# Optimization experiments

Hardware: AMD Instinct MI355X
Metric: run time of the kernel (lower is better)

The kernel has to match this reference:

```python
import jax, jax.numpy as jnp
import numpy as np

B, T, D = 2, 2048, 1024
N_HEADS = 16
HEAD_DIM = D // N_HEADS
HIDDEN = 4 * D
LN_EPS = 1e-6  # flax LayerNorm default


def apply_rotary_pos_emb(x, positions):
    # x: (B, T, H, head_dim); positions: (T,)
    head_dim = x.shape[-1]
    inv_freq = 1.0 / 10000 ** (jnp.arange(0, head_dim, 2).astype(jnp.float32) / head_dim)
    freqs = jnp.outer(positions.astype(jnp.float32), inv_freq)  # (T, head_dim//2)
    cos_emb = jnp.cos(freqs)[None, :, None, :]
    sin_emb = jnp.sin(freqs)[None, :, None, :]
    x1 = x[..., : head_dim // 2]
    x2 = x[..., head_dim // 2 :]
    return jnp.concatenate([x1 * cos_emb - x2 * sin_emb,
                            x1 * sin_emb + x2 * cos_emb], axis=-1)


def layernorm(x, scale, bias):
    mu = jnp.mean(x, axis=-1, keepdims=True)
    var = jnp.mean(jnp.square(x - mu), axis=-1, keepdims=True)
    return (x - mu) * jax.lax.rsqrt(var + LN_EPS) * scale + bias


def setup_inputs() -> dict:
    key = jax.random.key(0)
    ks = jax.random.split(key, 8)
    lecun = lambda k, shape: jax.random.normal(k, shape, jnp.float32) * (1.0 / np.sqrt(shape[0]))
    x = jax.random.normal(ks[0], (B, T, D), jnp.float32)
    positions = jnp.arange(T, dtype=jnp.int32)
    mask = jnp.tril(jnp.ones((T, T), dtype=bool))[None, None]  # causal (1,1,T,T)
    return {
        "x": x,
        "positions": positions,
        "mask": mask,
        "ln1_scale": jnp.ones((D,), jnp.float32),
        "ln1_bias": jnp.zeros((D,), jnp.float32),
        "w_qkv": lecun(ks[1], (D, 3 * D)),
        "w_o": lecun(ks[2], (D, D)),
        "ln2_scale": jnp.ones((D,), jnp.float32),
        "ln2_bias": jnp.zeros((D,), jnp.float32),
        "w1": lecun(ks[3], (D, HIDDEN)),
        "b1": jnp.zeros((HIDDEN,), jnp.float32),
        "w2": lecun(ks[4], (HIDDEN, D)),
        "b2": jnp.zeros((D,), jnp.float32),
    }


def reference(x, positions, mask, ln1_scale, ln1_bias, w_qkv, w_o,
              ln2_scale, ln2_bias, w1, b1, w2, b2):
    h = layernorm(x, ln1_scale, ln1_bias)
    qkv = h @ w_qkv  # (B,T,3D)
    qkv = qkv.reshape(B, T, 3, N_HEADS, HEAD_DIM)
    q, k, v = jnp.moveaxis(qkv, 2, 0)  # each (B,T,H,hd)
    q = apply_rotary_pos_emb(q, positions)
    k = apply_rotary_pos_emb(k, positions)
    q = jnp.transpose(q, (0, 2, 1, 3))  # (B,H,T,hd)
    k = jnp.transpose(k, (0, 2, 1, 3))
    v = jnp.transpose(v, (0, 2, 1, 3))
    scale = 1.0 / jnp.sqrt(jnp.float32(HEAD_DIM))
    attn_weights = jnp.einsum('bhqd,bhkd->bhqk', q, k) * scale
    attn_weights = jnp.where(mask, attn_weights, -1e10)
    attn_weights = jax.nn.softmax(attn_weights, axis=-1)
    h = jnp.einsum('bhqk,bhkd->bhqd', attn_weights, v)
    h = jnp.transpose(h, (0, 2, 1, 3)).reshape(B, T, D)
    h = h @ w_o
    x = x + h
    h = layernorm(x, ln2_scale, ln2_bias)
    h = jax.nn.gelu(h @ w1 + b1)  # approximate gelu, matching flax nn.gelu default
    h = h @ w2 + b2
    return x + h
```

## Files before the change

kernel.cpp:

```cpp
#include <hip/hip_runtime.h>


typedef __bf16 bf16_t;
typedef bf16_t bf16x8 __attribute__((ext_vector_type(8)));
typedef float f32x4 __attribute__((ext_vector_type(4)));

#define M_ROWS 4096
#define DMODEL 1024
#define TSEQ   2048
#define NHEAD  16
#define HDIM   64

__device__ __forceinline__ ushort f2bf(float f) {
  union { float f; unsigned u; } v; v.f = f;
  unsigned r = (v.u + 0x7fffu + ((v.u >> 16) & 1u)) >> 16;
  return (ushort)r;
}
__device__ __forceinline__ float bf2f(ushort u) {
  union { unsigned u; float f; } v; v.u = ((unsigned)u) << 16;
  return v.f;
}
__device__ __forceinline__ unsigned cvt_pk_bf16(float a, float b) {
  unsigned r;
  asm("v_cvt_pk_bf16_f32 %0, %1, %2" : "=v"(r) : "v"(a), "v"(b));
  return r;
}
__device__ __forceinline__ void gload_lds16(const void* g, void* l) {
  __builtin_amdgcn_global_load_lds(
      (const __attribute__((address_space(1))) unsigned*)g,
      (__attribute__((address_space(3))) unsigned*)l, 16, 0, 0);
}
__device__ __forceinline__ f32x4 mfma16(bf16x8 a, bf16x8 b, f32x4 c) {
  return __builtin_amdgcn_mfma_f32_16x16x32_bf16(a, b, c, 0, 0, 0);
}
__device__ __forceinline__ float gelu_f(float x) {
  float y = 0.7978845608028654f * (x + 0.044715f * x * x * x);
  float e = __expf(2.0f * y);
  float t = 1.0f - 2.0f / (e + 1.0f);
  return 0.5f * x * (1.0f + t);
}

__global__ __launch_bounds__(256)
void transpose_bf16(const float* __restrict__ src, ushort* __restrict__ dst,
                    int K, int N) {
  __shared__ float t[32][33];
  int n0 = blockIdx.x * 32, k0 = blockIdx.y * 32;
  int tx = threadIdx.x & 31, ty = threadIdx.x >> 5;
#pragma unroll
  for (int i = 0; i < 4; i++) {
    int k = ty + i * 8;
    t[k][tx] = src[(size_t)(k0 + k) * N + n0 + tx];
  }
  __syncthreads();
#pragma unroll
  for (int i = 0; i < 4; i++) {
    int nn = ty + i * 8;
    dst[(size_t)(n0 + nn) * K + k0 + tx] = f2bf(t[tx][nn]);
  }
}

__global__ __launch_bounds__(256)
void ln_kernel(const float* __restrict__ x, const float* __restrict__ sc,
               const float* __restrict__ bi, ushort* __restrict__ out) {
  int row = blockIdx.x;
  int tid = threadIdx.x;
  const float4 v = *(const float4*)&x[(size_t)row * DMODEL + tid * 4];
  float s = v.x + v.y + v.z + v.w;
  float s2 = v.x * v.x + v.y * v.y + v.z * v.z + v.w * v.w;
#pragma unroll
  for (int off = 32; off > 0; off >>= 1) {
    s += __shfl_down(s, off);
    s2 += __shfl_down(s2, off);
  }
  __shared__ float red[8];
  int lane = tid & 63, w = tid >> 6;
  if (lane == 0) { red[w * 2] = s; red[w * 2 + 1] = s2; }
  __syncthreads();
  float S = red[0] + red[2] + red[4] + red[6];
  float S2 = red[1] + red[3] + red[5] + red[7];
  float mu = S * (1.0f / DMODEL);
  float var = S2 * (1.0f / DMODEL) - mu * mu;
  float rs = rsqrtf(var + 1e-6f);
  float4 scv = *(const float4*)&sc[tid * 4];
  float4 biv = *(const float4*)&bi[tid * 4];
  ushort4 o;
  o.x = f2bf((v.x - mu) * rs * scv.x + biv.x);
  o.y = f2bf((v.y - mu) * rs * scv.y + biv.y);
  o.z = f2bf((v.z - mu) * rs * scv.z + biv.z);
  o.w = f2bf((v.w - mu) * rs * scv.w + biv.w);
  *(ushort4*)&out[(size_t)row * DMODEL + tid * 4] = o;
}

__global__ __launch_bounds__(256)
void rope_table(const int* __restrict__ positions, float2* __restrict__ tab) {
  int i = blockIdx.x * 256 + threadIdx.x;
  int t = i >> 5, f = i & 31;
  float inv = __expf(-(float)f * (1.0f / 32.0f) * 9.210340371976184f);
  float a = (float)positions[t] * inv;
  tab[i] = make_float2(cosf(a), sinf(a));
}

__global__ __launch_bounds__(256)
void rope_apply(const ushort* __restrict__ qkv, const float2* __restrict__ tab,
                ushort* __restrict__ Q, ushort* __restrict__ Kd,
                ushort* __restrict__ VT) {
  __shared__ ushort vt[64][66];
  int t0 = blockIdx.x * 64;
  int bh = blockIdx.y;
  int b = bh >> 4, h = bh & 15;
  int f = threadIdx.x & 31, tg = threadIdx.x >> 5;
#pragma unroll
  for (int i = 0; i < 8; i++) {
    int tt = tg * 8 + i;
    int t = t0 + tt;
    const ushort* qr = qkv + (size_t)(b * TSEQ + t) * 3072 + h * 64 + f;
    float2 cs = tab[t * 32 + f];
    float c = cs.x, s = cs.y;
    float q1 = bf2f(qr[0]),    q2 = bf2f(qr[32]);
    float k1 = bf2f(qr[1024]), k2 = bf2f(qr[1056]);
    ushort* Qp = Q + ((size_t)bh * TSEQ + t) * HDIM;
    ushort* Kp = Kd + ((size_t)bh * TSEQ + t) * HDIM;
    Qp[f]      = f2bf(q1 * c - q2 * s);
    Qp[f + 32] = f2bf(q1 * s + q2 * c);
    Kp[f]      = f2bf(k1 * c - k2 * s);
    Kp[f + 32] = f2bf(k1 * s + k2 * c);
    vt[f][tt]      = qr[2048];
    vt[f + 32][tt] = qr[2080];
  }
  __syncthreads();
  int t = threadIdx.x & 63, fg = threadIdx.x >> 6;
  ushort* Vp = VT + (size_t)bh * HDIM * TSEQ + t0 + t;
#pragma unroll
  for (int j = 0; j < 16; j++) {
    int ff = fg * 16 + j;
    Vp[(size_t)ff * TSEQ] = vt[ff][t];
  }
}

__global__ __launch_bounds__(256, 4)
void attn_kernel(const ushort* __restrict__ Q, const ushort* __restrict__ Kd,
                 const ushort* __restrict__ VT, ushort* __restrict__ O) {
  int bh = blockIdx.x;
  int qb = 31 - (int)blockIdx.y;
  int nt = qb + 1;
  int tid = threadIdx.x;
  int lane = tid & 63, w = tid >> 6;
  int qw = qb * 64 + w * 16;
  int lr = lane & 15, lg = lane >> 4;
  int q_abs = qw + lr;

  const ushort* Qb = Q + (size_t)bh * TSEQ * HDIM;
  const ushort* Kb = Kd + (size_t)bh * TSEQ * HDIM;
  const ushort* Vb = VT + (size_t)bh * HDIM * TSEQ;

  __shared__ ushort lK[2][64 * 64];
  __shared__ ushort lV[2][64 * 64];
  __shared__ ushort pt[4][16 * 64];
  ushort* myp = pt[w];

  int srow0 = tid >> 3, sch = tid & 7;

  auto stage = [&](int buf, int kt) {
#pragma unroll
    for (int c = 0; c < 2; c++) {
      int r = c * 32 + srow0;
      int gch = sch ^ (r & 7);
      gload_lds16(Kb + (size_t)(kt + r) * HDIM + gch * 8,
                  &lK[buf][c * 2048 + tid * 8]);
      gload_lds16(Vb + (size_t)r * TSEQ + kt + gch * 8,
                  &lV[buf][c * 2048 + tid * 8]);
    }
  };

  const float QS = 0.125f * 1.44269504088896340736f;
  bf16x8 aq0 = *(const bf16x8*)&Qb[(size_t)q_abs * HDIM + lg * 8];
  bf16x8 aq1 = *(const bf16x8*)&Qb[(size_t)q_abs * HDIM + 32 + lg * 8];
#pragma unroll
  for (int j = 0; j < 8; j++) {
    aq0[j] = (bf16_t)((float)aq0[j] * QS);
    aq1[j] = (bf16_t)((float)aq1[j] * QS);
  }

  float m_run = -1e30f, l_run = 0.0f;
  f32x4 o[4] = {};

  stage(0, 0);
  __syncthreads();

  for (int it = 0; it < nt; ++it) {
    int kt = it * 64;
    int buf = it & 1;
    bool diag = (it == nt - 1);

    if (it + 1 < nt) stage(buf ^ 1, kt + 64);

    f32x4 sa[4];
#pragma unroll
    for (int cb = 0; cb < 4; cb++) {
      int row = cb * 16 + lr;
      const ushort* kp = &lK[buf][row * 64];
      bf16x8 k0 = *(const bf16x8*)(kp + (((lg    ) ^ (row & 7)) << 3));
      bf16x8 k1 = *(const bf16x8*)(kp + (((lg + 4) ^ (row & 7)) << 3));
      f32x4 z = {};
      z = mfma16(k0, aq0, z);
      sa[cb] = mfma16(k1, aq1, z);
    }

    if (diag) {
#pragma unroll
      for (int cb = 0; cb < 4; cb++)
#pragma unroll
        for (int r = 0; r < 4; r++)
          if (kt + cb * 16 + lg * 4 + r > q_abs) sa[cb][r] = -1e30f;
    }

    f32x4 m4;
#pragma unroll
    for (int r = 0; r < 4; r++)
      m4[r] = fmaxf(fmaxf(sa[0][r], sa[1][r]), fmaxf(sa[2][r], sa[3][r]));
    float mx = fmaxf(fmaxf(m4[0], m4[1]), fmaxf(m4[2], m4[3]));
    mx = fmaxf(mx, __shfl_xor(mx, 16, 64));
    mx = fmaxf(mx, __shfl_xor(mx, 32, 64));
    float mn = fmaxf(m_run, mx);
    float rescale = __builtin_amdgcn_exp2f(m_run - mn);
    m_run = mn;

    float ps = 0.0f;
    uint2 pk[4];
#pragma unroll
    for (int cb = 0; cb < 4; cb++) {
      float p0 = __builtin_amdgcn_exp2f(sa[cb][0] - mn);
      float p1 = __builtin_amdgcn_exp2f(sa[cb][1] - mn);
      float p2 = __builtin_amdgcn_exp2f(sa[cb][2] - mn);
      float p3 = __builtin_amdgcn_exp2f(sa[cb][3] - mn);
      ps += (p0 + p1) + (p2 + p3);
      pk[cb].x = cvt_pk_bf16(p0, p1);
      pk[cb].y = cvt_pk_bf16(p2, p3);
    }
    ps += __shfl_xor(ps, 16, 64);
    ps += __shfl_xor(ps, 32, 64);
    l_run = l_run * rescale + ps;

#pragma unroll
    for (int cb = 0; cb < 4; cb++)
      *(uint2*)&myp[lr * 64 + (((cb * 4 + lg) ^ lr) << 2)] = pk[cb];

#pragma unroll
    for (int d = 0; d < 4; d++)
#pragma unroll
      for (int r = 0; r < 4; r++) o[d][r] *= rescale;

    union U8 { uint2 h[2]; bf16x8 v; };
    U8 t0, t1;
    t0.h[0] = *(const uint2*)&myp[lr * 64 + (((lg * 2    ) ^ lr) << 2)];
    t0.h[1] = *(const uint2*)&myp[lr * 64 + (((lg * 2 + 1) ^ lr) << 2)];
    t1.h[0] = *(const uint2*)&myp[lr * 64 + (((8 + lg * 2    ) ^ lr) << 2)];
    t1.h[1] = *(const uint2*)&myp[lr * 64 + (((8 + lg * 2 + 1) ^ lr) << 2)];

#pragma unroll
    for (int d = 0; d < 4; d++) {
      int row = d * 16 + lr;
      const ushort* vp = &lV[buf][row * 64];
      bf16x8 va0 = *(const bf16x8*)(vp + (((lg    ) ^ (row & 7)) << 3));
      bf16x8 va1 = *(const bf16x8*)(vp + (((lg + 4) ^ (row & 7)) << 3));
      o[d] = mfma16(va0, t0.v, o[d]);
      o[d] = mfma16(va1, t1.v, o[d]);
    }

    __syncthreads();
  }

  int b = bh >> 4, h = bh & 15;
  float linv = 1.0f / l_run;
  size_t obase = (size_t)(b * TSEQ + qw + lr) * DMODEL + h * 64;
#pragma unroll
  for (int d = 0; d < 4; d++) {
    uint2 st;
    st.x = cvt_pk_bf16(o[d][0] * linv, o[d][1] * linv);
    st.y = cvt_pk_bf16(o[d][2] * linv, o[d][3] * linv);
    *(uint2*)&O[obase + d * 16 + lg * 4] = st;
  }
}

template <int EPI, int BN>
__global__ __launch_bounds__(256)
void gemm_kernel(const ushort* __restrict__ A, const ushort* __restrict__ Bt,
                 void* __restrict__ Cout, const float* __restrict__ bias,
                 const float* __restrict__ resid, int M, int N, int K,
                 int nbn) {
  constexpr int NF = BN / 32;
  __shared__ ushort lA[2][128 * 64];
  __shared__ ushort lB[2][BN * 64];
  int tid = threadIdx.x;
  int lane = tid & 63, w = tid >> 6;
  int wm = w >> 1, wn = w & 1;

  int nwg = gridDim.x;
  int cpx = nwg >> 3;
  int wg = ((int)blockIdx.x & 7) * cpx + ((int)blockIdx.x >> 3);
  int bm = wg / nbn, bn = wg % nbn;

  f32x4 acc[4][NF] = {};

  const ushort* Ab = A + (size_t)bm * 128 * K;
  const ushort* Bb = Bt + (size_t)bn * BN * K;
  int lrow = lane & 15, lg = lane >> 4;
  int srow = tid >> 3, sch = tid & 7;

  auto stage = [&](int buf, int k0) {
#pragma unroll
    for (int c = 0; c < 4; c++) {
      int r = c * 32 + srow;
      int gch = sch ^ (r & 7);
      gload_lds16(Ab + (size_t)r * K + k0 + gch * 8,
                  &lA[buf][c * 2048 + tid * 8]);
    }
#pragma unroll
    for (int c = 0; c < NF; c++) {
      int r = c * 32 + srow;
      int gch = sch ^ (r & 7);
      gload_lds16(Bb + (size_t)r * K + k0 + gch * 8,
                  &lB[buf][c * 2048 + tid * 8]);
    }
  };

  int nt = K >> 6;
  stage(0, 0);
  __syncthreads();

  for (int t = 0; t < nt; ++t) {
    int cur = t & 1;

    bf16x8 af0[4], af1[4], bf0[NF], bf1[NF];
#pragma unroll
    for (int m = 0; m < 4; m++) {
      int row = wm * 64 + m * 16 + lrow;
      const ushort* p = &lA[cur][row * 64];
      af0[m] = *(const bf16x8*)(p + (((lg    ) ^ (row & 7)) << 3));
      af1[m] = *(const bf16x8*)(p + (((lg + 4) ^ (row & 7)) << 3));
    }
#pragma unroll
    for (int n = 0; n < NF; n++) {
      int row = wn * (BN / 2) + n * 16 + lrow;
      const ushort* p = &lB[cur][row * 64];
      bf0[n] = *(const bf16x8*)(p + (((lg    ) ^ (row & 7)) << 3));
      bf1[n] = *(const bf16x8*)(p + (((lg + 4) ^ (row & 7)) << 3));
    }

    if (t + 1 < nt) stage(cur ^ 1, (t + 1) << 6);

    __builtin_amdgcn_s_setprio(1);
#pragma unroll
    for (int m = 0; m < 4; m++)
#pragma unroll
      for (int n = 0; n < NF; n++)
        acc[m][n] = mfma16(af0[m], bf0[n], acc[m][n]);
#pragma unroll
    for (int m = 0; m < 4; m++)
#pragma unroll
      for (int n = 0; n < NF; n++)
        acc[m][n] = mfma16(af1[m], bf1[n], acc[m][n]);
    __builtin_amdgcn_s_setprio(0);

    __builtin_amdgcn_sched_barrier(0);
    asm volatile("s_waitcnt vmcnt(0)" ::: "memory");
    __builtin_amdgcn_s_barrier();
  }

#pragma unroll
  for (int m = 0; m < 4; m++) {
    int rbase = bm * 128 + wm * 64 + m * 16 + (lane >> 4) * 4;
#pragma unroll
    for (int n = 0; n < NF; n++) {
      int c = bn * BN + wn * (BN / 2) + n * 16 + (lane & 15);
#pragma unroll
      for (int r = 0; r < 4; r++) {
        float v = acc[m][n][r];
        size_t idx = (size_t)(rbase + r) * N + c;
        if constexpr (EPI == 0) {
          ((ushort*)Cout)[idx] = f2bf(v);
        } else if constexpr (EPI == 1) {
          ((float*)Cout)[idx] = v + resid[idx];
        } else if constexpr (EPI == 2) {
          ((ushort*)Cout)[idx] = f2bf(gelu_f(v + bias[c]));
        } else {
          ((float*)Cout)[idx] = v + bias[c] + resid[idx];
        }
      }
    }
  }
}

extern "C" void kernel_launch(void* const* d_in, const int* in_sizes, int n_in,
                              void* d_out, int out_size, void* d_ws,
                              size_t ws_size, hipStream_t stream) {
  const float* x      = (const float*)d_in[0];
  const int* positions = (const int*)d_in[1];
  const float* ln1_s  = (const float*)d_in[3];
  const float* ln1_b  = (const float*)d_in[4];
  const float* w_qkv  = (const float*)d_in[5];
  const float* w_o    = (const float*)d_in[6];
  const float* ln2_s  = (const float*)d_in[7];
  const float* ln2_b  = (const float*)d_in[8];
  const float* w1     = (const float*)d_in[9];
  const float* b1     = (const float*)d_in[10];
  const float* w2     = (const float*)d_in[11];
  const float* b2     = (const float*)d_in[12];
  float* out = (float*)d_out;

  char* ws = (char*)d_ws;
  size_t off = 0;
  auto nxt = [&](size_t bytes) {
    char* p = ws + off;
    off += (bytes + 255) & ~(size_t)255;
    return p;
  };
  ushort* wqkvT = (ushort*)nxt(3072ULL * 1024 * 2);
  ushort* woT   = (ushort*)nxt(1024ULL * 1024 * 2);
  ushort* w1T   = (ushort*)nxt(4096ULL * 1024 * 2);
  ushort* w2T   = (ushort*)nxt(1024ULL * 4096 * 2);
  ushort* h1    = (ushort*)nxt((size_t)M_ROWS * DMODEL * 2);
  ushort* qkv   = (ushort*)nxt((size_t)M_ROWS * 3072 * 2);
  ushort* Qb    = (ushort*)nxt(2ULL * NHEAD * TSEQ * HDIM * 2);
  ushort* Kb    = (ushort*)nxt(2ULL * NHEAD * TSEQ * HDIM * 2);
  ushort* VTb   = (ushort*)nxt(2ULL * NHEAD * TSEQ * HDIM * 2);
  ushort* attn  = (ushort*)nxt((size_t)M_ROWS * DMODEL * 2);
  float*  x2    = (float*)nxt((size_t)M_ROWS * DMODEL * 4);
  ushort* h2    = (ushort*)nxt((size_t)M_ROWS * DMODEL * 2);
  ushort* mid   = (ushort*)nxt((size_t)M_ROWS * 4096 * 2);
  float2* tab   = (float2*)nxt((size_t)TSEQ * 32 * 8);

  transpose_bf16<<<dim3(3072 / 32, 1024 / 32), 256, 0, stream>>>(w_qkv, wqkvT, 1024, 3072);
  transpose_bf16<<<dim3(1024 / 32, 1024 / 32), 256, 0, stream>>>(w_o, woT, 1024, 1024);
  transpose_bf16<<<dim3(4096 / 32, 1024 / 32), 256, 0, stream>>>(w1, w1T, 1024, 4096);
  transpose_bf16<<<dim3(1024 / 32, 4096 / 32), 256, 0, stream>>>(w2, w2T, 4096, 1024);
  rope_table<<<(TSEQ * 32) / 256, 256, 0, stream>>>(positions, tab);
  ln_kernel<<<M_ROWS, 256, 0, stream>>>(x, ln1_s, ln1_b, h1);
  gemm_kernel<0, 128><<<768, 256, 0, stream>>>(h1, wqkvT, qkv, nullptr, nullptr, 4096, 3072, 1024, 24);
  rope_apply<<<dim3(TSEQ / 64, 2 * NHEAD), 256, 0, stream>>>(qkv, tab, Qb, Kb, VTb);
  attn_kernel<<<dim3(32, 32), 256, 0, stream>>>(Qb, Kb, VTb, attn);
  gemm_kernel<1, 64><<<512, 256, 0, stream>>>(attn, woT, x2, nullptr, x, 4096, 1024, 1024, 16);
  ln_kernel<<<M_ROWS, 256, 0, stream>>>(x2, ln2_s, ln2_b, h2);
  gemm_kernel<2, 128><<<1024, 256, 0, stream>>>(h2, w1T, mid, b1, nullptr, 4096, 4096, 1024, 32);
  gemm_kernel<3, 64><<<512, 256, 0, stream>>>(mid, w2T, out, b2, x2, 4096, 1024, 4096, 16);
}
```

Before: 232.0 us.

## Add 256x256 tile GEMM with 512 threads for QKV and FFN1 projections

```diff
diff --git a/kernel.cpp b/kernel.cpp
--- a/kernel.cpp
+++ b/kernel.cpp
@@ -279,6 +279,126 @@
     st.x = cvt_pk_bf16(o[d][0] * linv, o[d][1] * linv);
     st.y = cvt_pk_bf16(o[d][2] * linv, o[d][3] * linv);
     *(uint2*)&O[obase + d * 16 + lg * 4] = st;
+  }
+}
+
+template <int EPI>
+__global__ __launch_bounds__(512)
+void gemm256(const ushort* __restrict__ A, const ushort* __restrict__ Bt,
+             void* __restrict__ Cout, const float* __restrict__ bias,
+             const float* __restrict__ resid, int M, int N, int K, int nbn) {
+  extern __shared__ ushort smem[];
+  ushort* lA = smem;
+  ushort* lB = smem + 32768;
+
+  int tid = threadIdx.x;
+  int lane = tid & 63, w = tid >> 6;
+  int wm = w >> 2, wn = w & 3;
+  int lrow = lane & 15, lg = lane >> 4;
+
+  int nwg = gridDim.x;
+  int cpx = nwg >> 3;
+  int wg = ((int)blockIdx.x & 7) * cpx + ((int)blockIdx.x >> 3);
+  int bm = wg / nbn, bn = wg % nbn;
+
+  const ushort* Ab = A + (size_t)bm * 256 * K;
+  const ushort* Bb = Bt + (size_t)bn * 256 * K;
+  int srow = tid >> 3, sch = tid & 7;
+
+  auto stage = [&](int buf, int k0) {
+#pragma unroll
+    for (int c = 0; c < 4; c++) {
+      int r = c * 64 + srow;
+      int gch = sch ^ (r & 7);
+      gload_lds16(Ab + (size_t)r * K + k0 + gch * 8,
+                  &lA[buf * 16384 + c * 4096 + tid * 8]);
+    }
+#pragma unroll
+    for (int c = 0; c < 4; c++) {
+      int r = c * 64 + srow;
+      int gch = sch ^ (r & 7);
+      gload_lds16(Bb + (size_t)r * K + k0 + gch * 8,
+                  &lB[buf * 16384 + c * 4096 + tid * 8]);
+    }
+  };
+
+  f32x4 acc[8][4] = {};
+
+  int nt = K >> 6;
+  stage(0, 0);
+  __syncthreads();
+
+  for (int t = 0; t < nt; ++t) {
+    int cur = t & 1;
+    const ushort* la = &lA[cur * 16384];
+    const ushort* lb = &lB[cur * 16384];
+
+    bf16x8 af[8], bf[4];
+#pragma unroll
+    for (int m = 0; m < 8; m++) {
+      int row = wm * 128 + m * 16 + lrow;
+      af[m] = *(const bf16x8*)&la[row * 64 + ((lg ^ (row & 7)) << 3)];
+    }
+#pragma unroll
+    for (int n = 0; n < 4; n++) {
+      int row = wn * 64 + n * 16 + lrow;
+      bf[n] = *(const bf16x8*)&lb[row * 64 + ((lg ^ (row & 7)) << 3)];
+    }
+
+    if (t + 1 < nt) stage(cur ^ 1, (t + 1) << 6);
+
+    __builtin_amdgcn_s_setprio(1);
+#pragma unroll
+    for (int m = 0; m < 8; m++)
+#pragma unroll
+      for (int n = 0; n < 4; n++)
+        acc[m][n] = mfma16(af[m], bf[n], acc[m][n]);
+    __builtin_amdgcn_s_setprio(0);
+
+#pragma unroll
+    for (int m = 0; m < 8; m++) {
+      int row = wm * 128 + m * 16 + lrow;
+      af[m] = *(const bf16x8*)&la[row * 64 + (((4 + lg) ^ (row & 7)) << 3)];
+    }
+#pragma unroll
+    for (int n = 0; n < 4; n++) {
+      int row = wn * 64 + n * 16 + lrow;
+      bf[n] = *(const bf16x8*)&lb[row * 64 + (((4 + lg) ^ (row & 7)) << 3)];
+    }
+    __builtin_amdgcn_s_setprio(1);
+#pragma unroll
+    for (int m = 0; m < 8; m++)
+#pragma unroll
+      for (int n = 0; n < 4; n++)
+        acc[m][n] = mfma16(af[m], bf[n], acc[m][n]);
+    __builtin_amdgcn_s_setprio(0);
+
+    __builtin_amdgcn_sched_barrier(0);
+    asm volatile("s_waitcnt vmcnt(0)" ::: "memory");
+    __builtin_amdgcn_s_barrier();
+  }
+
+#pragma unroll
+  for (int m = 0; m < 8; m++) {
+    int rbase = bm * 256 + wm * 128 + m * 16 + lg * 4;
+#pragma unroll
+    for (int n = 0; n < 4; n++) {
+      int c = bn * 256 + wn * 64 + n * 16 + lrow;
+#pragma unroll
+      for (int r = 0; r < 4; r++) {
+        float v = acc[m][n][r];
+        size_t idx = (size_t)(rbase + r) * N + c;
+        if constexpr (EPI == 0) {
+          ((ushort*)Cout)[idx] = f2bf(v);
+        } else if constexpr (EPI == 1) {
+          ((float*)Cout)[idx] = v + resid[idx];
+        } else if constexpr (EPI == 2) {
+          ((ushort*)Cout)[idx] = f2bf(gelu_f(v + bias[c]));
+        } else {
+          ((float*)Cout)[idx] = v + bias[c] + resid[idx];
+        }
+      }
+    }
   }
 }
 
@@ -430,17 +550,22 @@
   ushort* mid   = (ushort*)nxt((size_t)M_ROWS * 4096 * 2);
   float2* tab   = (float2*)nxt((size_t)TSEQ * 32 * 8);
 
+  (void)hipFuncSetAttribute((const void*)gemm256<0>,
+                            hipFuncAttributeMaxDynamicSharedMemorySize, 131072);
+  (void)hipFuncSetAttribute((const void*)gemm256<2>,
+                            hipFuncAttributeMaxDynamicSharedMemorySize, 131072);
+
   transpose_bf16<<<dim3(3072 / 32, 1024 / 32), 256, 0, stream>>>(w_qkv, wqkvT, 1024, 3072);
   transpose_bf16<<<dim3(1024 / 32, 1024 / 32), 256, 0, stream>>>(w_o, woT, 1024, 1024);
   transpose_bf16<<<dim3(4096 / 32, 1024 / 32), 256, 0, stream>>>(w1, w1T, 1024, 4096);
   transpose_bf16<<<dim3(1024 / 32, 4096 / 32), 256, 0, stream>>>(w2, w2T, 4096, 1024);
   rope_table<<<(TSEQ * 32) / 256, 256, 0, stream>>>(positions, tab);
   ln_kernel<<<M_ROWS, 256, 0, stream>>>(x, ln1_s, ln1_b, h1);
-  gemm_kernel<0, 128><<<768, 256, 0, stream>>>(h1, wqkvT, qkv, nullptr, nullptr, 4096, 3072, 1024, 24);
+  gemm256<0><<<192, 512, 131072, stream>>>(h1, wqkvT, qkv, nullptr, nullptr, 4096, 3072, 1024, 12);
   rope_apply<<<dim3(TSEQ / 64, 2 * NHEAD), 256, 0, stream>>>(qkv, tab, Qb, Kb, VTb);
   attn_kernel<<<dim3(32, 32), 256, 0, stream>>>(Qb, Kb, VTb, attn);
   gemm_kernel<1, 64><<<512, 256, 0, stream>>>(attn, woT, x2, nullptr, x, 4096, 1024, 1024, 16);
   ln_kernel<<<M_ROWS, 256, 0, stream>>>(x2, ln2_s, ln2_b, h2);
-  gemm_kernel<2, 128><<<1024, 256, 0, stream>>>(h2, w1T, mid, b1, nullptr, 4096, 4096, 1024, 32);
+  gemm256<2><<<256, 512, 131072, stream>>>(h2, w1T, mid, b1, nullptr, 4096, 4096, 1024, 16);
   gemm_kernel<3, 64><<<512, 256, 0, stream>>>(mid, w2T, out, b2, x2, 4096, 1024, 4096, 16);
 }
```

Result: faster. 224.2 us (-3.3%).

## Deepen GEMM pipeline to four K=32 LDS stages with prefetch distance two

Applied to the files above, without the earlier changes.

```diff
diff --git a/kernel.cpp b/kernel.cpp
--- a/kernel.cpp
+++ b/kernel.cpp
@@ -289,8 +289,9 @@
                  const float* __restrict__ resid, int M, int N, int K,
                  int nbn) {
   constexpr int NF = BN / 32;
-  __shared__ ushort lA[2][128 * 64];
-  __shared__ ushort lB[2][BN * 64];
+  constexpr int VC = 2 + BN / 64;
+  __shared__ ushort lA[4][128 * 32];
+  __shared__ ushort lB[4][BN * 32];
   int tid = threadIdx.x;
   int lane = tid & 63, w = tid >> 6;
   int wm = w >> 1, wn = w & 1;
@@ -305,66 +306,63 @@
   const ushort* Ab = A + (size_t)bm * 128 * K;
   const ushort* Bb = Bt + (size_t)bn * BN * K;
   int lrow = lane & 15, lg = lane >> 4;
-  int srow = tid >> 3, sch = tid & 7;
+  int srow = tid >> 2, sch = tid & 3;
 
   auto stage = [&](int buf, int k0) {
 #pragma unroll
-    for (int c = 0; c < 4; c++) {
-      int r = c * 32 + srow;
-      int gch = sch ^ (r & 7);
+    for (int c = 0; c < 2; c++) {
+      int r = c * 64 + srow;
+      int gch = sch ^ ((r >> 1) & 3);
       gload_lds16(Ab + (size_t)r * K + k0 + gch * 8,
                   &lA[buf][c * 2048 + tid * 8]);
     }
 #pragma unroll
-    for (int c = 0; c < NF; c++) {
-      int r = c * 32 + srow;
-      int gch = sch ^ (r & 7);
+    for (int c = 0; c < BN / 64; c++) {
+      int r = c * 64 + srow;
+      int gch = sch ^ ((r >> 1) & 3);
       gload_lds16(Bb + (size_t)r * K + k0 + gch * 8,
                   &lB[buf][c * 2048 + tid * 8]);
     }
   };
 
-  int nt = K >> 6;
+  int nt = K >> 5;
   stage(0, 0);
-  __syncthreads();
+  stage(1, 32);
 
   for (int t = 0; t < nt; ++t) {
-    int cur = t & 1;
-
-    bf16x8 af0[4], af1[4], bf0[NF], bf1[NF];
+    int cur = t & 3;
+
+    if (t < nt - 1) {
+      if constexpr (BN == 128)
+        asm volatile("s_waitcnt vmcnt(4)" ::: "memory");
+      else
+        asm volatile("s_waitcnt vmcnt(3)" ::: "memory");
+    } else {
+      asm volatile("s_waitcnt vmcnt(0)" ::: "memory");
+    }
+    __builtin_amdgcn_s_barrier();
+
+    if (t + 2 < nt) stage((t + 2) & 3, (t + 2) << 5);
+
+    bf16x8 af[4], bfr[NF];
 #pragma unroll
     for (int m = 0; m < 4; m++) {
       int row = wm * 64 + m * 16 + lrow;
-      const ushort* p = &lA[cur][row * 64];
-      af0[m] = *(const bf16x8*)(p + (((lg    ) ^ (row & 7)) << 3));
-      af1[m] = *(const bf16x8*)(p + (((lg + 4) ^ (row & 7)) << 3));
+      af[m] = *(const bf16x8*)&lA[cur][row * 32 + ((lg ^ ((row >> 1) & 3)) << 3)];
     }
 #pragma unroll
     for (int n = 0; n < NF; n++) {
       int row = wn * (BN / 2) + n * 16 + lrow;
-      const ushort* p = &lB[cur][row * 64];
-      bf0[n] = *(const bf16x8*)(p + (((lg    ) ^ (row & 7)) << 3));
-      bf1[n] = *(const bf16x8*)(p + (((lg + 4) ^ (row & 7)) << 3));
-    }
-
-    if (t + 1 < nt) stage(cur ^ 1, (t + 1) << 6);
+      bfr[n] = *(const bf16x8*)&lB[cur][row * 32 + ((lg ^ ((row >> 1) & 3)) << 3)];
+    }
 
     __builtin_amdgcn_s_setprio(1);
 #pragma unroll
     for (int m = 0; m < 4; m++)
 #pragma unroll
       for (int n = 0; n < NF; n++)
-        acc[m][n] = mfma16(af0[m], bf0[n], acc[m][n]);
-#pragma unroll
-    for (int m = 0; m < 4; m++)
-#pragma unroll
-      for (int n = 0; n < NF; n++)
-        acc[m][n] = mfma16(af1[m], bf1[n], acc[m][n]);
+        acc[m][n] = mfma16(af[m], bfr[n], acc[m][n]);
     __builtin_amdgcn_s_setprio(0);
-
-    __builtin_amdgcn_sched_barrier(0);
-    asm volatile("s_waitcnt vmcnt(0)" ::: "memory");
-    __builtin_amdgcn_s_barrier();
   }
 
 #pragma unroll
```

After: 280.4 us. 1.21x slower.
